# Optimization experiments

Measured on AMD Instinct MI355X. Metric: run time of the kernel, lower is better.

The kernel has to match this reference:

```python
import jax, jax.numpy as jnp
import numpy as np

B, N, C = 8, 1024, 768
HEADS = 8
HD = C // HEADS  # head_dim = qk_dim // num_heads since qk_ratio=1
SCALE = HD ** (-0.5)


def setup_inputs() -> dict:
    key = jax.random.key(0)
    ks = jax.random.split(key, 8)
    s = 0.02
    return {
        "x": jax.random.normal(ks[0], (B, N, C), dtype=jnp.float32),
        "y": jax.random.normal(ks[1], (B, N, C), dtype=jnp.float32),
        "relative_pos": jax.random.normal(ks[2], (HEADS, N, N), dtype=jnp.float32),
        "H": 32,
        "W": 32,
        "Wq": jax.random.normal(ks[3], (C, C), dtype=jnp.float32) * s,
        "Wk": jax.random.normal(ks[4], (C, C), dtype=jnp.float32) * s,
        "Wv": jax.random.normal(ks[5], (C, C), dtype=jnp.float32) * s,
        "Wp": jax.random.normal(ks[6], (C, C), dtype=jnp.float32) * s,
        "bp": jnp.zeros((C,), dtype=jnp.float32),
    }


def reference(x, y, relative_pos, H, W, Wq, Wk, Wv, Wp, bp):
    # sr_ratio == 1 path: K/V come directly from y (no spatial reduction).
    b, n, c = x.shape
    q = (x @ Wq.T).reshape(b, n, HEADS, HD)       # bnhd
    k = (y @ Wk.T).reshape(b, n, HEADS, HD)       # bmhd
    v = (y @ Wv.T).reshape(b, n, HEADS, HD)       # bmhd
    # scores: QK^T * scale + learned relative position bias (broadcast over batch)
    attn = jnp.einsum("bnhd,bmhd->bhnm", q, k) * SCALE + relative_pos[None]
    attn = jax.nn.softmax(attn, axis=-1)
    out = jnp.einsum("bhnm,bmhd->bnhd", attn, v).reshape(b, n, c)
    return out @ Wp.T + bp
```

## Files before the change

### kernel.cpp

```cpp
#include <hip/hip_runtime.h>
#include <hip/hip_bf16.h>
#include <cstdint>
#include <cstddef>


using f32x4  = __attribute__((ext_vector_type(4))) float;
using bf16x8 = __attribute__((ext_vector_type(8))) __bf16;

constexpr int Bb = 8, Nn = 1024, Cc = 768;
constexpr float LOG2E = 1.4426950408889634f;
constexpr float QSC   = 0.10206207261596575f * 1.4426950408889634f;

__device__ __forceinline__ uint16_t f2bf(float f) {
  union { float f; uint32_t u; } v; v.f = f;
  return (uint16_t)((v.u + 0x7fffu + ((v.u >> 16) & 1u)) >> 16);
}

__device__ __forceinline__ void gl_lds16(const void* g, void* l) {
  __builtin_amdgcn_global_load_lds(
      (const __attribute__((address_space(1))) void*)g,
      (__attribute__((address_space(3))) void*)l, 16, 0, 0);
}

__device__ __forceinline__ f32x4 mfma16(bf16x8 a, bf16x8 b, f32x4 c) {
  return __builtin_amdgcn_mfma_f32_16x16x32_bf16(a, b, c, 0, 0, 0);
}

template <int CTRL>
__device__ __forceinline__ float dpp_add(float v) {
  union { float f; int i; } u, r;
  u.f = v;
  r.i = __builtin_amdgcn_update_dpp(u.i, u.i, CTRL, 0xF, 0xF, false);
  return v + r.f;
}
__device__ __forceinline__ float red16_add(float v) {
  v = dpp_add<0x128>(v);
  v = dpp_add<0x124>(v);
  v = dpp_add<0x122>(v);
  v = dpp_add<0x121>(v);
  return v;
}

constexpr int NX4 = (Bb * Nn * Cc) / 4;
constexpr int NW4 = (Cc * Cc) / 4;
__global__ void cvt_all(const float* __restrict__ x, const float* __restrict__ y,
                        const float* __restrict__ wq, const float* __restrict__ wk,
                        const float* __restrict__ wv, const float* __restrict__ wp,
                        uint16_t* __restrict__ xb, uint16_t* __restrict__ yb,
                        uint16_t* __restrict__ dq, uint16_t* __restrict__ dk,
                        uint16_t* __restrict__ dv, uint16_t* __restrict__ dp) {
  int i = blockIdx.x * blockDim.x + threadIdx.x;
  const float* s; uint16_t* d; int off; float sc = 1.f;
  if (i < NX4) {
    s = x; d = xb; off = i;
  } else if (i < 2 * NX4) {
    s = y; d = yb; off = i - NX4;
  } else {
    int j = i - 2 * NX4;
    int wsel = j / NW4;
    off = j - wsel * NW4;
    switch (wsel) {
      case 0:  s = wq; d = dq; sc = QSC; break;
      case 1:  s = wk; d = dk; break;
      case 2:  s = wv; d = dv; break;
      default: s = wp; d = dp; break;
    }
  }
  float4 v = ((const float4*)s)[off];
  ushort4 o;
  o.x = f2bf(v.x * sc); o.y = f2bf(v.y * sc);
  o.z = f2bf(v.z * sc); o.w = f2bf(v.w * sc);
  ((ushort4*)d)[off] = o;
}

__device__ __forceinline__ void gemm_core(const uint16_t* __restrict__ A,
                                          const uint16_t* __restrict__ Bt,
                                          uint16_t* As, uint16_t* Bs,
                                          int m0, int n0, f32x4 (&acc)[4][4]) {
  const int tid = threadIdx.x;
  const int lane = tid & 63, l16 = lane & 15, quad = lane >> 4;
  const int w = tid >> 6;
  const int wm = (w & 1) * 64, wn = (w >> 1) * 64;

  int soff[4];
#pragma unroll
  for (int i = 0; i < 4; ++i) {
    int idx = tid + 256 * i;
    int row = idx >> 3, pc = idx & 7;
    int c = pc ^ (row & 7);
    soff[i] = row * 768 + c * 8;
  }

  for (int k0 = 0; k0 < 768; k0 += 64) {
    __syncthreads();
#pragma unroll
    for (int i = 0; i < 4; ++i)
      gl_lds16(A + (size_t)m0 * 768 + k0 + soff[i], &As[(tid + 256 * i) * 8]);
#pragma unroll
    for (int i = 0; i < 4; ++i)
      gl_lds16(Bt + (size_t)n0 * 768 + k0 + soff[i], &Bs[(tid + 256 * i) * 8]);
    __syncthreads();

#pragma unroll
    for (int ks = 0; ks < 2; ++ks) {
      bf16x8 a[4], b[4];
      const int phys = (ks * 4 + quad) ^ (l16 & 7);
#pragma unroll
      for (int i = 0; i < 4; ++i)
        a[i] = *(const bf16x8*)&As[(wm + i * 16 + l16) * 64 + phys * 8];
#pragma unroll
      for (int j = 0; j < 4; ++j)
        b[j] = *(const bf16x8*)&Bs[(wn + j * 16 + l16) * 64 + phys * 8];
#pragma unroll
      for (int i = 0; i < 4; ++i)
#pragma unroll
        for (int j = 0; j < 4; ++j)
          acc[i][j] = mfma16(a[i], b[j], acc[i][j]);
    }
  }
}

__global__ __launch_bounds__(256, 2) void qkv_kernel(
    const uint16_t* __restrict__ xb, const uint16_t* __restrict__ yb,
    const uint16_t* __restrict__ wq, const uint16_t* __restrict__ wk,
    const uint16_t* __restrict__ wv, uint16_t* __restrict__ Qb,
    uint16_t* __restrict__ Kb, uint16_t* __restrict__ Vt) {
  __shared__ uint16_t smem[24576];
  const int id = blockIdx.x;
  const int xcd = id & 7, jj = id >> 3;
  const int mt = xcd * 8 + (jj & 7);
  const int rest = jj >> 3;
  const int kind = rest / 6, nb = rest % 6;
  const int m0 = mt * 128, n0 = nb * 128;

  const int tid = threadIdx.x, lane = tid & 63;
  const int l16 = lane & 15, quad = lane >> 4, w = tid >> 6;
  const int wm = (w & 1) * 64, wn = (w >> 1) * 64;

  if (kind == 0) {
    f32x4 acc[4][4] = {};
    gemm_core(xb, wq, smem, smem + 8192, m0, n0, acc);
#pragma unroll
    for (int i = 0; i < 4; ++i)
#pragma unroll
      for (int j = 0; j < 4; ++j) {
        int col = n0 + wn + j * 16 + l16;
#pragma unroll
        for (int r = 0; r < 4; ++r) {
          int row = m0 + wm + i * 16 + quad * 4 + r;
          Qb[(size_t)row * 768 + col] = f2bf(acc[i][j][r]);
        }
      }
    return;
  }

  uint16_t* As = smem;
  uint16_t* Bk = smem + 8192;
  uint16_t* Bv = smem + 16384;

  int soff[4];
#pragma unroll
  for (int i = 0; i < 4; ++i) {
    int idx = tid + 256 * i;
    int row = idx >> 3, pc = idx & 7;
    soff[i] = row * 768 + (pc ^ (row & 7)) * 8;
  }

  f32x4 ak[4][4] = {}, av[4][4] = {};
  for (int k0 = 0; k0 < 768; k0 += 64) {
    __syncthreads();
#pragma unroll
    for (int i = 0; i < 4; ++i)
      gl_lds16(yb + (size_t)m0 * 768 + k0 + soff[i], &As[(tid + 256 * i) * 8]);
#pragma unroll
    for (int i = 0; i < 4; ++i)
      gl_lds16(wk + (size_t)n0 * 768 + k0 + soff[i], &Bk[(tid + 256 * i) * 8]);
#pragma unroll
    for (int i = 0; i < 4; ++i)
      gl_lds16(wv + (size_t)n0 * 768 + k0 + soff[i], &Bv[(tid + 256 * i) * 8]);
    __syncthreads();

#pragma unroll
    for (int ks = 0; ks < 2; ++ks) {
      bf16x8 a[4], bk[4], bv[4];
      const int phys = (ks * 4 + quad) ^ (l16 & 7);
#pragma unroll
      for (int i = 0; i < 4; ++i)
        a[i] = *(const bf16x8*)&As[(wm + i * 16 + l16) * 64 + phys * 8];
#pragma unroll
      for (int j = 0; j < 4; ++j) {
        bk[j] = *(const bf16x8*)&Bk[(wn + j * 16 + l16) * 64 + phys * 8];
        bv[j] = *(const bf16x8*)&Bv[(wn + j * 16 + l16) * 64 + phys * 8];
      }
#pragma unroll
      for (int i = 0; i < 4; ++i)
#pragma unroll
        for (int j = 0; j < 4; ++j) {
          ak[i][j] = mfma16(a[i], bk[j], ak[i][j]);
          av[i][j] = mfma16(a[i], bv[j], av[i][j]);
        }
    }
  }

#pragma unroll
  for (int i = 0; i < 4; ++i)
#pragma unroll
    for (int j = 0; j < 4; ++j) {
      int col = n0 + wn + j * 16 + l16;
#pragma unroll
      for (int r = 0; r < 4; ++r) {
        int row = m0 + wm + i * 16 + quad * 4 + r;
        Kb[(size_t)row * 768 + col] = f2bf(ak[i][j][r]);
      }
    }

  __syncthreads();
#pragma unroll
  for (int i = 0; i < 4; ++i)
#pragma unroll
    for (int j = 0; j < 4; ++j) {
      int ml = wm + i * 16 + quad * 4;
      int nl = wn + j * 16 + l16;
      ushort4 pk;
      pk.x = f2bf(av[i][j][0]); pk.y = f2bf(av[i][j][1]);
      pk.z = f2bf(av[i][j][2]); pk.w = f2bf(av[i][j][3]);
      *(ushort4*)&smem[nl * 130 + ml] = pk;
    }
  __syncthreads();
  const int bidx = m0 >> 10, nseq0 = m0 & 1023;
#pragma unroll
  for (int pass = 0; pass < 8; ++pass) {
    int nl = pass * 16 + (tid >> 4);
    int col = n0 + nl;
    int h = col / 96, hd = col % 96;
    int m = (tid & 15) * 8;
    bf16x8 v = *(const bf16x8*)&smem[nl * 130 + m];
    size_t o = (((size_t)(bidx * 8 + h) * 96 + hd) << 10) + nseq0 + m;
    *(bf16x8*)(Vt + o) = v;
  }
}

__global__ __launch_bounds__(256, 3) void proj_kernel(
    const uint16_t* __restrict__ A, const uint16_t* __restrict__ Bt,
    float* __restrict__ out, const float* __restrict__ bias) {
  __shared__ uint16_t smem[16384];
  const int id = blockIdx.x;
  const int xcd = id & 7, jj = id >> 3;
  const int mt = xcd * 8 + (jj & 7);
  const int nb = jj >> 3;
  const int m0 = mt * 128, n0 = nb * 128;
  const int tid = threadIdx.x, lane = tid & 63;
  const int l16 = lane & 15, quad = lane >> 4, w = tid >> 6;
  const int wm = (w & 1) * 64, wn = (w >> 1) * 64;

  f32x4 acc[4][4] = {};
  gemm_core(A, Bt, smem, smem + 8192, m0, n0, acc);

  float bv[4];
#pragma unroll
  for (int j = 0; j < 4; ++j) bv[j] = bias[n0 + wn + j * 16 + l16];
#pragma unroll
  for (int i = 0; i < 4; ++i)
#pragma unroll
    for (int j = 0; j < 4; ++j) {
      int col = n0 + wn + j * 16 + l16;
#pragma unroll
      for (int r = 0; r < 4; ++r) {
        int row = m0 + wm + i * 16 + quad * 4 + r;
        out[(size_t)row * 768 + col] = acc[i][j][r] + bv[j];
      }
    }
}

__global__ __launch_bounds__(256, 2) void attn_kernel(
    const uint16_t* __restrict__ Q,
    const uint16_t* __restrict__ Kb,
    const uint16_t* __restrict__ Vt,
    const float* __restrict__ rel,
    uint16_t* __restrict__ AO) {
  __shared__ uint16_t Ks[2][64 * 96];
  __shared__ uint16_t Vs[2][96 * 64];
  __shared__ uint16_t Ps[128 * 64];

  const int tid = threadIdx.x;
  const int id = blockIdx.x;
  const int swz = (id & 7) * 64 + (id >> 3);
  const int h  = swz >> 6;
  const int q0 = ((swz >> 3) & 7) * 128;
  const int b  = swz & 7;
  const int bh = b * 8 + h;

  const int w = tid >> 6, lane = tid & 63;
  const int l16 = lane & 15, quad = lane >> 4;
  const int l7 = l16 & 7;

  bf16x8 qf[2][3];
#pragma unroll
  for (int st = 0; st < 2; ++st) {
    const int qrow = q0 + st * 64 + w * 16 + l16;
    const uint16_t* qp =
        Q + ((size_t)(b * 1024 + qrow)) * 768 + h * 96 + quad * 8;
#pragma unroll
    for (int j = 0; j < 3; ++j) qf[st][j] = *(const bf16x8*)(qp + j * 32);
  }

  auto kSrc = [](int c) {
    int r = c / 12, pc = c % 12;
    int kc = (pc < 8) ? (pc ^ (r & 7)) : (8 + ((pc & 3) ^ (r & 3)));
    return r * 768 + kc * 8;
  };
  auto vSrc = [](int c) {
    int d = c >> 3, pc = c & 7;
    return d * 1024 + (pc ^ (d & 7)) * 8;
  };
  int koffs[3], voffs[3];
#pragma unroll
  for (int i = 0; i < 3; ++i) {
    koffs[i] = kSrc(tid + 256 * i);
    voffs[i] = vSrc(tid + 256 * i);
  }

  const uint16_t* kslab = Kb + ((size_t)(b * 1024)) * 768 + h * 96;
  const uint16_t* vslab = Vt + ((size_t)(bh * 96) << 10);
  const float* relbase0 =
      rel + ((size_t)h << 20) + ((size_t)(q0 + w * 16 + quad * 4) << 10) + l16;
  const float* relbase1 = relbase0 + (64 << 10);

  auto stage = [&](int knext, int bufi) {
    const uint16_t* kb = kslab + (size_t)knext * 768;
    const uint16_t* vb = vslab + knext;
    uint16_t* Kbuf = &Ks[bufi][0];
    uint16_t* Vbuf = &Vs[bufi][0];
#pragma unroll
    for (int i = 0; i < 3; ++i) {
      gl_lds16(kb + koffs[i], Kbuf + (tid + 256 * i) * 8);
      gl_lds16(vb + voffs[i], Vbuf + (tid + 256 * i) * 8);
    }
  };

  float relv[2][16];
  auto loadrel = [&](int knext) {
#pragma unroll
    for (int r = 0; r < 4; ++r)
#pragma unroll
      for (int nt = 0; nt < 4; ++nt) {
        relv[0][nt * 4 + r] = relbase0[(size_t)r * 1024 + knext + nt * 16];
        relv[1][nt * 4 + r] = relbase1[(size_t)r * 1024 + knext + nt * 16];
      }
  };

  float l_i[2][4] = {};
  f32x4 o_acc[2][6] = {};

  stage(0, 0);
  loadrel(0);

#pragma unroll 2
  for (int kt = 0; kt < 16; ++kt) {
    const int cur = kt & 1, nxt = (kt + 1) & 1;
    __syncthreads();
    if (kt < 15) stage((kt + 1) * 64, nxt);
    const uint16_t* KsC = &Ks[cur][0];
    const uint16_t* VsC = &Vs[cur][0];

    f32x4 s[2][4] = {};
    __builtin_amdgcn_s_setprio(1);
#pragma unroll
    for (int ksi = 0; ksi < 3; ++ksi) {
#pragma unroll
      for (int nt = 0; nt < 4; ++nt) {
        const int row = nt * 16 + l16;
        const int c = ksi * 4 + quad;
        const int phys =
            (ksi < 2) ? (c ^ (row & 7)) : (8 + ((c & 3) ^ (row & 3)));
        bf16x8 kf = *(const bf16x8*)&KsC[row * 96 + phys * 8];
        s[0][nt] = mfma16(qf[0][ksi], kf, s[0][nt]);
        s[1][nt] = mfma16(qf[1][ksi], kf, s[1][nt]);
      }
    }
    __builtin_amdgcn_s_setprio(0);

    const int khi = l16 >> 3;
#pragma unroll
    for (int st = 0; st < 2; ++st) {
      float pv[16];
#pragma unroll
      for (int nt = 0; nt < 4; ++nt)
#pragma unroll
        for (int r = 0; r < 4; ++r)
          pv[nt * 4 + r] = __builtin_amdgcn_exp2f(
              fmaf(relv[st][nt * 4 + r], LOG2E, s[st][nt][r]));
#pragma unroll
      for (int r = 0; r < 4; ++r)
        l_i[st][r] += (pv[r] + pv[4 + r]) + (pv[8 + r] + pv[12 + r]);
#pragma unroll
      for (int r = 0; r < 4; ++r) {
        const int qloc = quad * 4 + r;
        const int rowoff = (st * 64 + w * 16 + qloc) * 64;
        const int sw = qloc & 7;
#pragma unroll
        for (int nt = 0; nt < 4; ++nt) {
          const int kc = 2 * nt + khi;
          Ps[rowoff + (((kc ^ sw) << 3) | l7)] = f2bf(pv[nt * 4 + r]);
        }
      }
    }

    if (kt < 15) loadrel((kt + 1) * 64);

    asm volatile("s_waitcnt lgkmcnt(0)" ::: "memory");

    __builtin_amdgcn_s_setprio(1);
#pragma unroll
    for (int ksi = 0; ksi < 2; ++ksi) {
      const int phys = (ksi * 4 + quad) ^ l7;
      bf16x8 pf0 = *(const bf16x8*)&Ps[(w * 16 + l16) * 64 + phys * 8];
      bf16x8 pf1 = *(const bf16x8*)&Ps[(64 + w * 16 + l16) * 64 + phys * 8];
#pragma unroll
      for (int jt = 0; jt < 6; ++jt) {
        const int d = jt * 16 + l16;
        bf16x8 vf = *(const bf16x8*)&VsC[d * 64 + phys * 8];
        o_acc[0][jt] = mfma16(pf0, vf, o_acc[0][jt]);
        o_acc[1][jt] = mfma16(pf1, vf, o_acc[1][jt]);
      }
    }
    __builtin_amdgcn_s_setprio(0);
  }

#pragma unroll
  for (int st = 0; st < 2; ++st)
#pragma unroll
    for (int r = 0; r < 4; ++r) {
      float inv = 1.f / red16_add(l_i[st][r]);
      int row = q0 + st * 64 + w * 16 + quad * 4 + r;
#pragma unroll
      for (int jt = 0; jt < 6; ++jt) {
        int col = h * 96 + jt * 16 + l16;
        AO[(size_t)(b * 1024 + row) * 768 + col] = f2bf(o_acc[st][jt][r] * inv);
      }
    }
}

extern "C" void kernel_launch(void* const* d_in, const int* in_sizes, int n_in,
                              void* d_out, int out_size, void* d_ws,
                              size_t ws_size, hipStream_t stream) {
  const float* x   = (const float*)d_in[0];
  const float* y   = (const float*)d_in[1];
  const float* rel = (const float*)d_in[2];
  const float* Wq  = (const float*)d_in[5];
  const float* Wk  = (const float*)d_in[6];
  const float* Wv  = (const float*)d_in[7];
  const float* Wp  = (const float*)d_in[8];
  const float* bp  = (const float*)d_in[9];
  float* out = (float*)d_out;

  const size_t nBNC = (size_t)Bb * Nn * Cc;
  const size_t nW = (size_t)Cc * Cc;

  char* ws = (char*)d_ws;
  size_t off = 0;
  auto alloc = [&](size_t bytes) {
    char* p = ws + off;
    off += (bytes + 255) & ~(size_t)255;
    return p;
  };
  uint16_t* xb  = (uint16_t*)alloc(nBNC * 2);
  uint16_t* yb  = (uint16_t*)alloc(nBNC * 2);
  uint16_t* wqb = (uint16_t*)alloc(nW * 2);
  uint16_t* wkb = (uint16_t*)alloc(nW * 2);
  uint16_t* wvb = (uint16_t*)alloc(nW * 2);
  uint16_t* wpb = (uint16_t*)alloc(nW * 2);
  uint16_t* Qb  = (uint16_t*)alloc(nBNC * 2);
  uint16_t* Kb  = (uint16_t*)alloc(nBNC * 2);
  uint16_t* Vtb = (uint16_t*)alloc(nBNC * 2);
  uint16_t* AOb = (uint16_t*)alloc(nBNC * 2);

  const int cvtBlocks = (2 * NX4 + 4 * NW4) / 256;
  cvt_all<<<cvtBlocks, 256, 0, stream>>>(x, y, Wq, Wk, Wv, Wp, xb, yb, wqb,
                                         wkb, wvb, wpb);

  qkv_kernel<<<dim3(768), 256, 0, stream>>>(xb, yb, wqb, wkb, wvb, Qb, Kb,
                                            Vtb);

  attn_kernel<<<dim3(512), 256, 0, stream>>>(Qb, Kb, Vtb, rel, AOb);

  proj_kernel<<<dim3(384), 256, 0, stream>>>(AOb, wpb, out, bp);
}
```

Baseline: 234.3 us.

## Fuse fp32-to-bf16 conversion of x and y into the QKV GEMM loader

The separate x/y conversion pass is removed. The QKV kernel now reads fp32 activations directly, converts them to bf16 in registers, and stores them to LDS, prefetching the next K-tile into registers during compute. This avoids writing and re-reading two bf16 copies of the activations. In exchange, the A tile is reloaded in fp32 by every N-block (double the bytes per load), and it goes through register staging rather than the direct global-to-LDS path.

Result: slower. 242.2 us (+3.4%).

```diff
diff --git a/kernel.cpp b/kernel.cpp
--- a/kernel.cpp
+++ b/kernel.cpp
@@ -24,6 +24,14 @@
 
 __device__ __forceinline__ f32x4 mfma16(bf16x8 a, bf16x8 b, f32x4 c) {
   return __builtin_amdgcn_mfma_f32_16x16x32_bf16(a, b, c, 0, 0, 0);
+}
+
+__device__ __forceinline__ void ldcvtA(const float* p, ushort4& lo,
+                                       ushort4& hi) {
+  float4 f0 = ((const float4*)p)[0];
+  float4 f1 = ((const float4*)p)[1];
+  lo.x = f2bf(f0.x); lo.y = f2bf(f0.y); lo.z = f2bf(f0.z); lo.w = f2bf(f0.w);
+  hi.x = f2bf(f1.x); hi.y = f2bf(f1.y); hi.z = f2bf(f1.z); hi.w = f2bf(f1.w);
 }
 
 template <int CTRL>
@@ -41,30 +49,20 @@
   return v;
 }
 
-constexpr int NX4 = (Bb * Nn * Cc) / 4;
 constexpr int NW4 = (Cc * Cc) / 4;
-__global__ void cvt_all(const float* __restrict__ x, const float* __restrict__ y,
-                        const float* __restrict__ wq, const float* __restrict__ wk,
-                        const float* __restrict__ wv, const float* __restrict__ wp,
-                        uint16_t* __restrict__ xb, uint16_t* __restrict__ yb,
-                        uint16_t* __restrict__ dq, uint16_t* __restrict__ dk,
-                        uint16_t* __restrict__ dv, uint16_t* __restrict__ dp) {
+__global__ void cvt_w(const float* __restrict__ wq, const float* __restrict__ wk,
+                      const float* __restrict__ wv, const float* __restrict__ wp,
+                      uint16_t* __restrict__ dq, uint16_t* __restrict__ dk,
+                      uint16_t* __restrict__ dv, uint16_t* __restrict__ dp) {
   int i = blockIdx.x * blockDim.x + threadIdx.x;
-  const float* s; uint16_t* d; int off; float sc = 1.f;
-  if (i < NX4) {
-    s = x; d = xb; off = i;
-  } else if (i < 2 * NX4) {
-    s = y; d = yb; off = i - NX4;
-  } else {
-    int j = i - 2 * NX4;
-    int wsel = j / NW4;
-    off = j - wsel * NW4;
-    switch (wsel) {
-      case 0:  s = wq; d = dq; sc = QSC; break;
-      case 1:  s = wk; d = dk; break;
-      case 2:  s = wv; d = dv; break;
-      default: s = wp; d = dp; break;
-    }
+  int wsel = i / NW4;
+  int off = i - wsel * NW4;
+  const float* s; uint16_t* d; float sc = 1.f;
+  switch (wsel) {
+    case 0:  s = wq; d = dq; sc = QSC; break;
+    case 1:  s = wk; d = dk; break;
+    case 2:  s = wv; d = dv; break;
+    default: s = wp; d = dp; break;
   }
   float4 v = ((const float4*)s)[off];
   ushort4 o;
@@ -121,7 +119,7 @@
 }
 
 __global__ __launch_bounds__(256, 2) void qkv_kernel(
-    const uint16_t* __restrict__ xb, const uint16_t* __restrict__ yb,
+    const float* __restrict__ x, const float* __restrict__ y,
     const uint16_t* __restrict__ wq, const uint16_t* __restrict__ wk,
     const uint16_t* __restrict__ wv, uint16_t* __restrict__ Qb,
     uint16_t* __restrict__ Kb, uint16_t* __restrict__ Vt) {
@@ -137,9 +135,59 @@
   const int l16 = lane & 15, quad = lane >> 4, w = tid >> 6;
   const int wm = (w & 1) * 64, wn = (w >> 1) * 64;
 
+  int soff[4];
+#pragma unroll
+  for (int i = 0; i < 4; ++i) {
+    int idx = tid + 256 * i;
+    int row = idx >> 3, pc = idx & 7;
+    soff[i] = row * 768 + (pc ^ (row & 7)) * 8;
+  }
+
+  uint16_t* As = smem;
+  uint16_t* Bk = smem + 8192;
+  uint16_t* Bv = smem + 16384;
+
   if (kind == 0) {
+    const float* Ax = x + (size_t)m0 * 768;
+    ushort4 lo[4], hi[4];
+#pragma unroll
+    for (int i = 0; i < 4; ++i) ldcvtA(Ax + soff[i], lo[i], hi[i]);
+
     f32x4 acc[4][4] = {};
-    gemm_core(xb, wq, smem, smem + 8192, m0, n0, acc);
+    for (int k0 = 0; k0 < 768; k0 += 64) {
+      __syncthreads();
+#pragma unroll
+      for (int i = 0; i < 4; ++i) {
+        *(ushort4*)&As[(tid + 256 * i) * 8] = lo[i];
+        *(ushort4*)&As[(tid + 256 * i) * 8 + 4] = hi[i];
+      }
+#pragma unroll
+      for (int i = 0; i < 4; ++i)
+        gl_lds16(wq + (size_t)n0 * 768 + k0 + soff[i],
+                 &Bk[(tid + 256 * i) * 8]);
+      __syncthreads();
+      if (k0 + 64 < 768) {
+#pragma unroll
+        for (int i = 0; i < 4; ++i)
+          ldcvtA(Ax + k0 + 64 + soff[i], lo[i], hi[i]);
+      }
+#pragma unroll
+      for (int ks = 0; ks < 2; ++ks) {
+        bf16x8 a[4], b[4];
+        const int phys = (ks * 4 + quad) ^ (l16 & 7);
+#pragma unroll
+        for (int i = 0; i < 4; ++i)
+          a[i] = *(const bf16x8*)&As[(wm + i * 16 + l16) * 64 + phys * 8];
+#pragma unroll
+        for (int j = 0; j < 4; ++j)
+          b[j] = *(const bf16x8*)&Bk[(wn + j * 16 + l16) * 64 + phys * 8];
+#pragma unroll
+        for (int i = 0; i < 4; ++i)
+#pragma unroll
+          for (int j = 0; j < 4; ++j)
+            acc[i][j] = mfma16(a[i], b[j], acc[i][j]);
+      }
+    }
 #pragma unroll
     for (int i = 0; i < 4; ++i)
 #pragma unroll
@@ -154,24 +202,19 @@
     return;
   }
 
-  uint16_t* As = smem;
-  uint16_t* Bk = smem + 8192;
-  uint16_t* Bv = smem + 16384;
-
-  int soff[4];
-#pragma unroll
-  for (int i = 0; i < 4; ++i) {
-    int idx = tid + 256 * i;
-    int row = idx >> 3, pc = idx & 7;
-    soff[i] = row * 768 + (pc ^ (row & 7)) * 8;
-  }
+  const float* Ay = y + (size_t)m0 * 768;
+  ushort4 lo[4], hi[4];
+#pragma unroll
+  for (int i = 0; i < 4; ++i) ldcvtA(Ay + soff[i], lo[i], hi[i]);
 
   f32x4 ak[4][4] = {}, av[4][4] = {};
   for (int k0 = 0; k0 < 768; k0 += 64) {
     __syncthreads();
 #pragma unroll
-    for (int i = 0; i < 4; ++i)
-      gl_lds16(yb + (size_t)m0 * 768 + k0 + soff[i], &As[(tid + 256 * i) * 8]);
+    for (int i = 0; i < 4; ++i) {
+      *(ushort4*)&As[(tid + 256 * i) * 8] = lo[i];
+      *(ushort4*)&As[(tid + 256 * i) * 8 + 4] = hi[i];
+    }
 #pragma unroll
     for (int i = 0; i < 4; ++i)
       gl_lds16(wk + (size_t)n0 * 768 + k0 + soff[i], &Bk[(tid + 256 * i) * 8]);
@@ -179,7 +222,11 @@
     for (int i = 0; i < 4; ++i)
       gl_lds16(wv + (size_t)n0 * 768 + k0 + soff[i], &Bv[(tid + 256 * i) * 8]);
     __syncthreads();
-
+    if (k0 + 64 < 768) {
+#pragma unroll
+      for (int i = 0; i < 4; ++i)
+        ldcvtA(Ay + k0 + 64 + soff[i], lo[i], hi[i]);
+    }
 #pragma unroll
     for (int ks = 0; ks < 2; ++ks) {
       bf16x8 a[4], bk[4], bv[4];
@@ -464,8 +511,6 @@
     off += (bytes + 255) & ~(size_t)255;
     return p;
   };
-  uint16_t* xb  = (uint16_t*)alloc(nBNC * 2);
-  uint16_t* yb  = (uint16_t*)alloc(nBNC * 2);
   uint16_t* wqb = (uint16_t*)alloc(nW * 2);
   uint16_t* wkb = (uint16_t*)alloc(nW * 2);
   uint16_t* wvb = (uint16_t*)alloc(nW * 2);
@@ -475,12 +520,10 @@
   uint16_t* Vtb = (uint16_t*)alloc(nBNC * 2);
   uint16_t* AOb = (uint16_t*)alloc(nBNC * 2);
 
-  const int cvtBlocks = (2 * NX4 + 4 * NW4) / 256;
-  cvt_all<<<cvtBlocks, 256, 0, stream>>>(x, y, Wq, Wk, Wv, Wp, xb, yb, wqb,
-                                         wkb, wvb, wpb);
-
-  qkv_kernel<<<dim3(768), 256, 0, stream>>>(xb, yb, wqb, wkb, wvb, Qb, Kb,
-                                            Vtb);
+  cvt_w<<<dim3(4 * NW4 / 256), 256, 0, stream>>>(Wq, Wk, Wv, Wp, wqb, wkb,
+                                                 wvb, wpb);
+
+  qkv_kernel<<<dim3(768), 256, 0, stream>>>(x, y, wqb, wkb, wvb, Qb, Kb, Vtb);
 
   attn_kernel<<<dim3(512), 256, 0, stream>>>(Qb, Kb, Vtb, rel, AOb);
 
```
